# Kernel tuning notes

Measured on AMD Instinct MI355X. Metric: run time of the kernel, lower is better.

The kernel has to match this reference:

```python
import jax, jax.numpy as jnp
import numpy as np

B, H, S, D = 4, 16, 2048, 128

def setup_inputs() -> dict:
    key = jax.random.key(0)
    kq, kk, kv = jax.random.split(key, 3)
    q = jax.random.normal(kq, (B, H, S, D), dtype=jnp.float32)
    k = jax.random.normal(kk, (B, H, S, D), dtype=jnp.float32)
    v = jax.random.normal(kv, (B, H, S, D), dtype=jnp.float32)
    # causal mask: True = masked (upper triangle above the diagonal)
    mask = jnp.triu(jnp.ones((S, S), dtype=jnp.bool_), k=1)[None, None, :, :]
    return {"q": q, "k": k, "v": v, "mask": mask}

def reference(q, k, v, mask):
    head_dim = q.shape[-1]
    scale = 1.0 / jnp.sqrt(jnp.float32(head_dim))
    # scores: [B, H, Sq, Sk]
    scores = jnp.einsum('bhqd,bhkd->bhqk', q, k) * scale
    scores = jnp.where(mask, -jnp.inf, scores)
    attention_weights = jax.nn.softmax(scores, axis=-1)
    # dropout p=0.0 (eval): identity
    context_vectors = jnp.einsum('bhqk,bhkd->bhqd', attention_weights, v)
    return (context_vectors, attention_weights)
```

## Files before the change

kernel.cpp:

```cpp
#include <hip/hip_runtime.h>
#include <hip/hip_bf16.h>

#define S_LEN 2048
#define D_DIM 128
#define BH_N  64
#define BR    64
#define BC    64
#define NTILE (S_LEN / BC)
#define SCALE 0.08838834764831845f
#define SD    (S_LEN * D_DIM)
#define LSUM_BYTES (BH_N * S_LEN * 4)
#define WS_NEED (LSUM_BYTES + (size_t)BH_N * SD * 2)

typedef __attribute__((ext_vector_type(8)))  short short8;
typedef __attribute__((ext_vector_type(16))) float f32x16;
typedef __attribute__((ext_vector_type(4)))  float fv4;

__device__ __forceinline__ ushort f2bf(float f) {
  union { float f; unsigned u; } x; x.f = f;
  unsigned r = x.u + 0x7FFFu + ((x.u >> 16) & 1u);
  return (ushort)(r >> 16);
}

__device__ __forceinline__ short8 pack8(float4 a, float4 b) {
  short8 p;
  p[0] = (short)f2bf(a.x); p[1] = (short)f2bf(a.y);
  p[2] = (short)f2bf(a.z); p[3] = (short)f2bf(a.w);
  p[4] = (short)f2bf(b.x); p[5] = (short)f2bf(b.y);
  p[6] = (short)f2bf(b.z); p[7] = (short)f2bf(b.w);
  return p;
}

__global__ __launch_bounds__(256) void cvt_k_kernel(
    const float* __restrict__ k, ushort* __restrict__ kb) {
  size_t total = (size_t)BH_N * SD / 8;
  for (size_t i = (size_t)blockIdx.x * 256 + threadIdx.x; i < total;
       i += (size_t)gridDim.x * 256) {
    float4 a = *(const float4*)(k + i * 8);
    float4 b = *(const float4*)(k + i * 8 + 4);
    *(short8*)(kb + i * 8) = pack8(a, b);
  }
}

__device__ __forceinline__ void map_block_a(int bid, int& bh, int& qb) {
  int xcd  = bid & 7;
  int rest = bid >> 3;
  bh = (rest >> 5) * 8 + xcd;
  qb = (NTILE - 1) - (rest & 31);
}

template <bool KB16>
__global__ __launch_bounds__(256, 2) void attn_flash_kernel(
    const float* __restrict__ q, const float* __restrict__ k,
    const ushort* __restrict__ kb, const float* __restrict__ v,
    float* __restrict__ ctx, float* __restrict__ lsum_out) {
  __shared__ __align__(16) char klds[BC * 256];
  __shared__ __align__(16) char vtlds[D_DIM * 128];
  __shared__ __align__(16) char plds[BR * 128];
  __shared__ float lred[2][BR];

  const int tid  = threadIdx.x;
  const int lane = tid & 63;
  const int w    = tid >> 6;
  const int wq   = w >> 1, wk = w & 1;
  const int l31  = lane & 31, lhi = lane >> 5;

  int bh, qb;
  map_block_a(blockIdx.x, bh, qb);

  const float*  qbase  = q  + (size_t)bh * SD;
  const float*  kbase  = k  + (size_t)bh * SD;
  const ushort* kbbase = kb + (size_t)bh * SD;
  const float*  vbase  = v  + (size_t)bh * SD;

  short8 qf[8];
  {
    const float* qrow = qbase + (size_t)(qb * BR + wq * 32 + l31) * D_DIM;
    #pragma unroll
    for (int s = 0; s < 8; ++s) {
      int d0 = 16 * s + 8 * lhi;
      float4 a = *(const float4*)(qrow + d0);
      float4 b = *(const float4*)(qrow + d0 + 4);
      qf[s] = pack8(a, b);
    }
  }

  float4 kreg[8], vreg[8];
  short8 kreg16[4];

  auto load_k = [&](int kt) {
    int trow = tid >> 2, tc = tid & 3;
    if constexpr (KB16) {
      const ushort* src = kbbase + (size_t)(kt * BC + trow) * D_DIM;
      #pragma unroll
      for (int i = 0; i < 4; ++i)
        kreg16[i] = *(const short8*)(src + tc * 8 + i * 32);
    } else {
      const float* src = kbase + (size_t)(kt * BC + trow) * D_DIM;
      #pragma unroll
      for (int i = 0; i < 4; ++i) {
        int c0 = tc * 8 + i * 32;
        kreg[2 * i]     = *(const float4*)(src + c0);
        kreg[2 * i + 1] = *(const float4*)(src + c0 + 4);
      }
    }
  };
  auto write_k = [&]() {
    int trow = tid >> 2, tc = tid & 3;
    #pragma unroll
    for (int i = 0; i < 4; ++i) {
      int c0 = tc * 8 + i * 32;
      int off = (trow * 256 + c0 * 2) ^ ((trow & 7) << 4);
      if constexpr (KB16)
        *(short8*)(klds + off) = kreg16[i];
      else
        *(short8*)(klds + off) = pack8(kreg[2 * i], kreg[2 * i + 1]);
    }
  };
  auto load_v = [&](int kt) {
    int kp = tid & 31, dg = tid >> 5;
    const float* r0 = vbase + (size_t)(kt * BC + 2 * kp) * D_DIM + dg * 16;
    #pragma unroll
    for (int i = 0; i < 4; ++i) {
      vreg[i]     = *(const float4*)(r0 + 4 * i);
      vreg[4 + i] = *(const float4*)(r0 + D_DIM + 4 * i);
    }
  };
  auto write_v = [&]() {
    int kp = tid & 31, dg = tid >> 5;
    #pragma unroll
    for (int j = 0; j < 16; ++j) {
      int d = dg * 16 + j;
      float lo = vreg[j >> 2][j & 3];
      float hi = vreg[4 + (j >> 2)][j & 3];
      unsigned u = (unsigned)f2bf(lo) | ((unsigned)f2bf(hi) << 16);
      int off = (d * 128 + kp * 4) ^ ((d & 7) << 4);
      *(unsigned*)(vtlds + off) = u;
    }
  };

  auto compute_s = [&]() -> f32x16 {
    f32x16 acc;
    #pragma unroll
    for (int i = 0; i < 16; ++i) acc[i] = 0.f;
    int krow = wk * 32 + l31;
    int base = krow * 256;
    int swz  = (krow & 7) << 4;
    #pragma unroll
    for (int s = 0; s < 8; ++s) {
      int off = (base + 32 * s + 16 * lhi) ^ swz;
      short8 kf = *(const short8*)(klds + off);
      acc = __builtin_amdgcn_mfma_f32_32x32x16_bf16(qf[s], kf, acc, 0, 0, 0);
    }
    return acc;
  };

  float l_lane[16];
  f32x16 o0, o1;
  #pragma unroll
  for (int i = 0; i < 16; ++i) { l_lane[i] = 0.f; o0[i] = 0.f; o1[i] = 0.f; }

  load_k(0); load_v(0);

  for (int kt = 0; kt <= qb; ++kt) {
    write_k(); write_v();
    if (kt < qb) { load_k(kt + 1); load_v(kt + 1); }
    __syncthreads();

    f32x16 acc = compute_s();
    int kcol_l = wk * 32 + l31;
    int kcol = kt * BC + kcol_l;
    bool diag = (kt == qb);
    #pragma unroll
    for (int r = 0; r < 16; ++r) {
      int rl = wq * 32 + (r & 3) + 8 * (r >> 2) + 4 * lhi;
      int qrow = qb * BR + rl;
      float e = (diag && kcol > qrow) ? 0.f : __expf(acc[r] * SCALE);
      l_lane[r] += e;
      int poff = (rl * 128 + kcol_l * 2) ^ ((rl & 7) << 4);
      *(ushort*)(plds + poff) = f2bf(e);
    }
    __syncthreads();

    #pragma unroll
    for (int s = 0; s < 4; ++s) {
      int prow = wq * 32 + l31;
      int paoff = (prow * 128 + (16 * s + 8 * lhi) * 2) ^ ((prow & 7) << 4);
      short8 pa = *(const short8*)(plds + paoff);
      int kko = (16 * s + 8 * lhi) * 2;
      int d0 = wk * 64 + l31;
      int d1 = d0 + 32;
      int off0 = (d0 * 128 + kko) ^ ((d0 & 7) << 4);
      int off1 = (d1 * 128 + kko) ^ ((d1 & 7) << 4);
      short8 vb0 = *(const short8*)(vtlds + off0);
      short8 vb1 = *(const short8*)(vtlds + off1);
      o0 = __builtin_amdgcn_mfma_f32_32x32x16_bf16(pa, vb0, o0, 0, 0, 0);
      o1 = __builtin_amdgcn_mfma_f32_32x32x16_bf16(pa, vb1, o1, 0, 0, 0);
    }
    __syncthreads();
  }

  #pragma unroll
  for (int r = 0; r < 16; ++r) {
    float x = l_lane[r];
    x += __shfl_xor(x, 1);  x += __shfl_xor(x, 2);  x += __shfl_xor(x, 4);
    x += __shfl_xor(x, 8);  x += __shfl_xor(x, 16);
    l_lane[r] = x;
  }
  if (l31 == 0) {
    #pragma unroll
    for (int r = 0; r < 16; ++r) {
      int rl = wq * 32 + (r & 3) + 8 * (r >> 2) + 4 * lhi;
      lred[wk][rl] = l_lane[r];
    }
  }
  __syncthreads();

  if (tid < BR)
    lsum_out[(size_t)bh * S_LEN + qb * BR + tid] = lred[0][tid] + lred[1][tid];

  float inv_l[16];
  #pragma unroll
  for (int r = 0; r < 16; ++r) {
    int rl = wq * 32 + (r & 3) + 8 * (r >> 2) + 4 * lhi;
    inv_l[r] = 1.0f / (lred[0][rl] + lred[1][rl]);
  }
  #pragma unroll
  for (int r = 0; r < 16; ++r) {
    int rl = wq * 32 + (r & 3) + 8 * (r >> 2) + 4 * lhi;
    size_t obase = (size_t)(bh * S_LEN + qb * BR + rl) * D_DIM;
    ctx[obase + wk * 64 + l31]      = o0[r] * inv_l[r];
    ctx[obase + wk * 64 + 32 + l31] = o1[r] * inv_l[r];
  }
}

template <bool KB16>
__global__ __launch_bounds__(256) void attn_wts_stream_kernel(
    const float* __restrict__ q, const float* __restrict__ k,
    const ushort* __restrict__ kb, const float* __restrict__ lsum,
    float* __restrict__ wts) {
  const int tid  = threadIdx.x;
  const int lane = tid & 63;
  const int w    = tid >> 6;
  const int l31  = lane & 31, lhi = lane >> 5;

  int bh, panel;
  {
    int bid = blockIdx.x;
    int xcd = bid & 7, rest = bid >> 3;
    bh    = (rest >> 4) * 8 + xcd;
    panel = 15 - (rest & 15);
  }

  const int qrow0 = panel * 128 + w * 32;
  float* wbase = wts + ((size_t)bh * S_LEN + qrow0) * S_LEN;

  short8 qf[8];
  {
    const float* qrow = q + ((size_t)bh * S_LEN + qrow0 + l31) * D_DIM;
    #pragma unroll
    for (int s = 0; s < 8; ++s) {
      int d0 = 16 * s + 8 * lhi;
      float4 a = *(const float4*)(qrow + d0);
      float4 b = *(const float4*)(qrow + d0 + 4);
      qf[s] = pack8(a, b);
    }
  }

  float invl[16];
  #pragma unroll
  for (int r = 0; r < 16; ++r) {
    int rl = (r & 3) + 8 * (r >> 2) + 4 * lhi;
    invl[r] = 1.0f / lsum[(size_t)bh * S_LEN + qrow0 + rl];
  }

  const int qmax = qrow0 + 31;
  const int nkt  = qmax / 64 + 1;

  const ushort* kbb = kb + (size_t)bh * SD;
  const float*  kfb = k  + (size_t)bh * SD;

  for (int kt = 0; kt < nkt; ++kt) {
    f32x16 a0, a1;
    #pragma unroll
    for (int i = 0; i < 16; ++i) { a0[i] = 0.f; a1[i] = 0.f; }

    if constexpr (KB16) {
      const ushort* k0 = kbb + (size_t)(kt * 64 + l31) * D_DIM;
      const ushort* k1 = k0 + 32 * D_DIM;
      #pragma unroll
      for (int s8 = 0; s8 < 8; ++s8) {
        int d0 = 16 * s8 + 8 * lhi;
        short8 kf0 = *(const short8*)(k0 + d0);
        short8 kf1 = *(const short8*)(k1 + d0);
        a0 = __builtin_amdgcn_mfma_f32_32x32x16_bf16(qf[s8], kf0, a0, 0, 0, 0);
        a1 = __builtin_amdgcn_mfma_f32_32x32x16_bf16(qf[s8], kf1, a1, 0, 0, 0);
      }
    } else {
      const float* k0 = kfb + (size_t)(kt * 64 + l31) * D_DIM;
      const float* k1 = k0 + 32 * D_DIM;
      #pragma unroll
      for (int s8 = 0; s8 < 8; ++s8) {
        int d0 = 16 * s8 + 8 * lhi;
        short8 kf0 = pack8(*(const float4*)(k0 + d0), *(const float4*)(k0 + d0 + 4));
        short8 kf1 = pack8(*(const float4*)(k1 + d0), *(const float4*)(k1 + d0 + 4));
        a0 = __builtin_amdgcn_mfma_f32_32x32x16_bf16(qf[s8], kf0, a0, 0, 0, 0);
        a1 = __builtin_amdgcn_mfma_f32_32x32x16_bf16(qf[s8], kf1, a1, 0, 0, 0);
      }
    }

    const int kc0 = kt * 64 + l31;
    const int kc1 = kc0 + 32;
    #pragma unroll
    for (int r = 0; r < 16; ++r) {
      int qr = qrow0 + (r & 3) + 8 * (r >> 2) + 4 * lhi;
      a0[r] = (kc0 > qr) ? 0.f : __expf(a0[r] * SCALE) * invl[r];
      a1[r] = (kc1 > qr) ? 0.f : __expf(a1[r] * SCALE) * invl[r];
    }

    float* cbase = wbase + kt * 64 + lane;
    #pragma unroll
    for (int r = 0; r < 16; ++r) {
      float sA = __shfl(a1[r], lane ^ 32);
      float sB = __shfl(a0[r], lane ^ 32);
      float vA = lhi ? sA : a0[r];
      float vB = lhi ? a1[r] : sB;
      int rA = (r & 3) + 8 * (r >> 2);
      __builtin_nontemporal_store(vA, cbase + (size_t)rA * S_LEN);
      __builtin_nontemporal_store(vB, cbase + (size_t)(rA + 4) * S_LEN);
    }
  }

  fv4 z = (fv4)0.f;
  const int c0 = nkt * 64;
  for (int rr = 0; rr < 32; ++rr) {
    float* rowp = wbase + (size_t)rr * S_LEN;
    for (int c = c0 + lane * 4; c < S_LEN; c += 256)
      __builtin_nontemporal_store(z, (fv4*)(rowp + c));
  }
}

extern "C" void kernel_launch(void* const* d_in, const int* in_sizes, int n_in,
                              void* d_out, int out_size, void* d_ws, size_t ws_size,
                              hipStream_t stream) {
  const float* q = (const float*)d_in[0];
  const float* k = (const float*)d_in[1];
  const float* v = (const float*)d_in[2];
  float* ctx = (float*)d_out;
  float* wts = ctx + (size_t)BH_N * SD;
  float*  lsum = (float*)d_ws;
  ushort* kb16 = (ushort*)((char*)d_ws + LSUM_BYTES);

  const bool fast = ws_size >= WS_NEED;

  if (fast) {
    cvt_k_kernel<<<dim3(2048), dim3(256), 0, stream>>>(k, kb16);
    attn_flash_kernel<true><<<dim3(BH_N * NTILE), dim3(256), 0, stream>>>(
        q, k, kb16, v, ctx, lsum);
    attn_wts_stream_kernel<true><<<dim3(BH_N * 16), dim3(256), 0, stream>>>(
        q, k, kb16, lsum, wts);
  } else {
    attn_flash_kernel<false><<<dim3(BH_N * NTILE), dim3(256), 0, stream>>>(
        q, k, kb16, v, ctx, lsum);
    attn_wts_stream_kernel<false><<<dim3(BH_N * 16), dim3(256), 0, stream>>>(
        q, k, kb16, lsum, wts);
  }
}
```

Measured before the change: 560.8 us.

## Fuse flash context pass and weights streaming pass into one kernel per panel

Merges the flash-attention context kernel and the attention-weights streaming kernel into a single kernel. Each block handles a 128-row query panel with one warp per 32 rows, computes row sums and context first, then reuses the in-register Q fragments and row sums to write normalized weights. This removes the lsum workspace round-trip, one launch, and the second Q load. In exchange, each warp now computes all 64 key columns per tile, and the grid shrinks from 2048 to 1024 blocks, which lowers parallelism and can load-imbalance the causal panels.

```diff
diff --git a/kernel.cpp b/kernel.cpp
--- a/kernel.cpp
+++ b/kernel.cpp
@@ -4,13 +4,10 @@
 #define S_LEN 2048
 #define D_DIM 128
 #define BH_N  64
-#define BR    64
-#define BC    64
-#define NTILE (S_LEN / BC)
+#define NTILE 32
 #define SCALE 0.08838834764831845f
 #define SD    (S_LEN * D_DIM)
-#define LSUM_BYTES (BH_N * S_LEN * 4)
-#define WS_NEED (LSUM_BYTES + (size_t)BH_N * SD * 2)
+#define WS_NEED ((size_t)BH_N * SD * 2)
 
 typedef __attribute__((ext_vector_type(8)))  short short8;
 typedef __attribute__((ext_vector_type(16))) float f32x16;
@@ -42,40 +39,37 @@
   }
 }
 
-__device__ __forceinline__ void map_block_a(int bid, int& bh, int& qb) {
-  int xcd  = bid & 7;
-  int rest = bid >> 3;
-  bh = (rest >> 5) * 8 + xcd;
-  qb = (NTILE - 1) - (rest & 31);
-}
-
 template <bool KB16>
-__global__ __launch_bounds__(256, 2) void attn_flash_kernel(
+__global__ __launch_bounds__(256, 2) void attn_fused2_kernel(
     const float* __restrict__ q, const float* __restrict__ k,
     const ushort* __restrict__ kb, const float* __restrict__ v,
-    float* __restrict__ ctx, float* __restrict__ lsum_out) {
-  __shared__ __align__(16) char klds[BC * 256];
-  __shared__ __align__(16) char vtlds[D_DIM * 128];
-  __shared__ __align__(16) char plds[BR * 128];
-  __shared__ float lred[2][BR];
+    float* __restrict__ ctx, float* __restrict__ wts) {
+  __shared__ __align__(16) char klds[64 * 256];
+  __shared__ __align__(16) char vtlds[128 * 128];
+  __shared__ __align__(16) char plds[4 * 4096];
 
   const int tid  = threadIdx.x;
   const int lane = tid & 63;
   const int w    = tid >> 6;
-  const int wq   = w >> 1, wk = w & 1;
   const int l31  = lane & 31, lhi = lane >> 5;
 
-  int bh, qb;
-  map_block_a(blockIdx.x, bh, qb);
-
-  const float*  qbase  = q  + (size_t)bh * SD;
+  int bh, panel;
+  {
+    int bid = blockIdx.x;
+    int xcd = bid & 7, rest = bid >> 3;
+    bh    = (rest >> 4) * 8 + xcd;
+    panel = 15 - (rest & 15);
+  }
+  const int qrow0 = panel * 128 + w * 32;
+  char* pw = plds + w * 4096;
+
   const float*  kbase  = k  + (size_t)bh * SD;
   const ushort* kbbase = kb + (size_t)bh * SD;
   const float*  vbase  = v  + (size_t)bh * SD;
 
   short8 qf[8];
   {
-    const float* qrow = qbase + (size_t)(qb * BR + wq * 32 + l31) * D_DIM;
+    const float* qrow = q + ((size_t)bh * S_LEN + qrow0 + l31) * D_DIM;
     #pragma unroll
     for (int s = 0; s < 8; ++s) {
       int d0 = 16 * s + 8 * lhi;
@@ -91,12 +85,12 @@
   auto load_k = [&](int kt) {
     int trow = tid >> 2, tc = tid & 3;
     if constexpr (KB16) {
-      const ushort* src = kbbase + (size_t)(kt * BC + trow) * D_DIM;
+      const ushort* src = kbbase + (size_t)(kt * 64 + trow) * D_DIM;
       #pragma unroll
       for (int i = 0; i < 4; ++i)
         kreg16[i] = *(const short8*)(src + tc * 8 + i * 32);
     } else {
-      const float* src = kbase + (size_t)(kt * BC + trow) * D_DIM;
+      const float* src = kbase + (size_t)(kt * 64 + trow) * D_DIM;
       #pragma unroll
       for (int i = 0; i < 4; ++i) {
         int c0 = tc * 8 + i * 32;
@@ -119,7 +113,7 @@
   };
   auto load_v = [&](int kt) {
     int kp = tid & 31, dg = tid >> 5;
-    const float* r0 = vbase + (size_t)(kt * BC + 2 * kp) * D_DIM + dg * 16;
+    const float* r0 = vbase + (size_t)(kt * 64 + 2 * kp) * D_DIM + dg * 16;
     #pragma unroll
     for (int i = 0; i < 4; ++i) {
       vreg[i]     = *(const float4*)(r0 + 4 * i);
@@ -139,146 +133,83 @@
     }
   };
 
-  auto compute_s = [&]() -> f32x16 {
-    f32x16 acc;
-    #pragma unroll
-    for (int i = 0; i < 16; ++i) acc[i] = 0.f;
-    int krow = wk * 32 + l31;
-    int base = krow * 256;
-    int swz  = (krow & 7) << 4;
-    #pragma unroll
-    for (int s = 0; s < 8; ++s) {
-      int off = (base + 32 * s + 16 * lhi) ^ swz;
-      short8 kf = *(const short8*)(klds + off);
-      acc = __builtin_amdgcn_mfma_f32_32x32x16_bf16(qf[s], kf, acc, 0, 0, 0);
-    }
-    return acc;
-  };
-
   float l_lane[16];
-  f32x16 o0, o1;
+  f32x16 o0, o1, o2, o3;
   #pragma unroll
-  for (int i = 0; i < 16; ++i) { l_lane[i] = 0.f; o0[i] = 0.f; o1[i] = 0.f; }
-
+  for (int i = 0; i < 16; ++i) {
+    l_lane[i] = 0.f; o0[i] = 0.f; o1[i] = 0.f; o2[i] = 0.f; o3[i] = 0.f;
+  }
+
+  const int nkt_blk = 2 * panel + 2;
   load_k(0); load_v(0);
 
-  for (int kt = 0; kt <= qb; ++kt) {
+  for (int kt = 0; kt < nkt_blk; ++kt) {
     write_k(); write_v();
-    if (kt < qb) { load_k(kt + 1); load_v(kt + 1); }
+    if (kt + 1 < nkt_blk) { load_k(kt + 1); load_v(kt + 1); }
     __syncthreads();
 
-    f32x16 acc = compute_s();
-    int kcol_l = wk * 32 + l31;
-    int kcol = kt * BC + kcol_l;
-    bool diag = (kt == qb);
-    #pragma unroll
-    for (int r = 0; r < 16; ++r) {
-      int rl = wq * 32 + (r & 3) + 8 * (r >> 2) + 4 * lhi;
-      int qrow = qb * BR + rl;
-      float e = (diag && kcol > qrow) ? 0.f : __expf(acc[r] * SCALE);
-      l_lane[r] += e;
-      int poff = (rl * 128 + kcol_l * 2) ^ ((rl & 7) << 4);
-      *(ushort*)(plds + poff) = f2bf(e);
+    if (kt * 64 <= qrow0 + 31) {
+      f32x16 a0, a1;
+      #pragma unroll
+      for (int i = 0; i < 16; ++i) { a0[i] = 0.f; a1[i] = 0.f; }
+      const int swz = (l31 & 7) << 4;
+      #pragma unroll
+      for (int s8 = 0; s8 < 8; ++s8) {
+        int c = 32 * s8 + 16 * lhi;
+        short8 kf0 = *(const short8*)(klds + ((l31 * 256 + c) ^ swz));
+        short8 kf1 = *(const short8*)(klds + (((l31 + 32) * 256 + c) ^ swz));
+        a0 = __builtin_amdgcn_mfma_f32_32x32x16_bf16(qf[s8], kf0, a0, 0, 0, 0);
+        a1 = __builtin_amdgcn_mfma_f32_32x32x16_bf16(qf[s8], kf1, a1, 0, 0, 0);
+      }
+      const int kc0 = kt * 64 + l31, kc1 = kc0 + 32;
+      #pragma unroll
+      for (int r = 0; r < 16; ++r) {
+        int rl = (r & 3) + 8 * (r >> 2) + 4 * lhi;
+        int qr = qrow0 + rl;
+        float e0 = (kc0 > qr) ? 0.f : __expf(a0[r] * SCALE);
+        float e1 = (kc1 > qr) ? 0.f : __expf(a1[r] * SCALE);
+        l_lane[r] += e0 + e1;
+        int swzr = (rl & 7) << 4;
+        *(ushort*)(pw + ((rl * 128 + l31 * 2) ^ swzr))      = f2bf(e0);
+        *(ushort*)(pw + ((rl * 128 + 64 + l31 * 2) ^ swzr)) = f2bf(e1);
+      }
+      #pragma unroll
+      for (int s = 0; s < 4; ++s) {
+        int kko = (16 * s + 8 * lhi) * 2;
+        short8 pa = *(const short8*)(pw + ((l31 * 128 + kko) ^ ((l31 & 7) << 4)));
+        short8 vb0 = *(const short8*)(vtlds + (((0 * 32 + l31) * 128 + kko) ^ ((l31 & 7) << 4)));
+        short8 vb1 = *(const short8*)(vtlds + (((1 * 32 + l31) * 128 + kko) ^ (((32 + l31) & 7) << 4)));
+        short8 vb2 = *(const short8*)(vtlds + (((2 * 32 + l31) * 128 + kko) ^ (((64 + l31) & 7) << 4)));
+        short8 vb3 = *(const short8*)(vtlds + (((3 * 32 + l31) * 128 + kko) ^ (((96 + l31) & 7) << 4)));
+        o0 = __builtin_amdgcn_mfma_f32_32x32x16_bf16(pa, vb0, o0, 0, 0, 0);
+        o1 = __builtin_amdgcn_mfma_f32_32x32x16_bf16(pa, vb1, o1, 0, 0, 0);
+        o2 = __builtin_amdgcn_mfma_f32_32x32x16_bf16(pa, vb2, o2, 0, 0, 0);
+        o3 = __builtin_amdgcn_mfma_f32_32x32x16_bf16(pa, vb3, o3, 0, 0, 0);
+      }
     }
     __syncthreads();
-
-    #pragma unroll
-    for (int s = 0; s < 4; ++s) {
-      int prow = wq * 32 + l31;
-      int paoff = (prow * 128 + (16 * s + 8 * lhi) * 2) ^ ((prow & 7) << 4);
-      short8 pa = *(const short8*)(plds + paoff);
-      int kko = (16 * s + 8 * lhi) * 2;
-      int d0 = wk * 64 + l31;
-      int d1 = d0 + 32;
-      int off0 = (d0 * 128 + kko) ^ ((d0 & 7) << 4);
-      int off1 = (d1 * 128 + kko) ^ ((d1 & 7) << 4);
-      short8 vb0 = *(const short8*)(vtlds + off0);
-      short8 vb1 = *(const short8*)(vtlds + off1);
-      o0 = __builtin_amdgcn_mfma_f32_32x32x16_bf16(pa, vb0, o0, 0, 0, 0);
-      o1 = __builtin_amdgcn_mfma_f32_32x32x16_bf16(pa, vb1, o1, 0, 0, 0);
-    }
-    __syncthreads();
-  }
-
+  }
+
+  float inv_l[16];
   #pragma unroll
   for (int r = 0; r < 16; ++r) {
     float x = l_lane[r];
     x += __shfl_xor(x, 1);  x += __shfl_xor(x, 2);  x += __shfl_xor(x, 4);
     x += __shfl_xor(x, 8);  x += __shfl_xor(x, 16);
-    l_lane[r] = x;
-  }
-  if (l31 == 0) {
-    #pragma unroll
-    for (int r = 0; r < 16; ++r) {
-      int rl = wq * 32 + (r & 3) + 8 * (r >> 2) + 4 * lhi;
-      lred[wk][rl] = l_lane[r];
-    }
-  }
-  __syncthreads();
-
-  if (tid < BR)
-    lsum_out[(size_t)bh * S_LEN + qb * BR + tid] = lred[0][tid] + lred[1][tid];
-
-  float inv_l[16];
-  #pragma unroll
-  for (int r = 0; r < 16; ++r) {
-    int rl = wq * 32 + (r & 3) + 8 * (r >> 2) + 4 * lhi;
-    inv_l[r] = 1.0f / (lred[0][rl] + lred[1][rl]);
-  }
-  #pragma unroll
-  for (int r = 0; r < 16; ++r) {
-    int rl = wq * 32 + (r & 3) + 8 * (r >> 2) + 4 * lhi;
-    size_t obase = (size_t)(bh * S_LEN + qb * BR + rl) * D_DIM;
-    ctx[obase + wk * 64 + l31]      = o0[r] * inv_l[r];
-    ctx[obase + wk * 64 + 32 + l31] = o1[r] * inv_l[r];
-  }
-}
-
-template <bool KB16>
-__global__ __launch_bounds__(256) void attn_wts_stream_kernel(
-    const float* __restrict__ q, const float* __restrict__ k,
-    const ushort* __restrict__ kb, const float* __restrict__ lsum,
-    float* __restrict__ wts) {
-  const int tid  = threadIdx.x;
-  const int lane = tid & 63;
-  const int w    = tid >> 6;
-  const int l31  = lane & 31, lhi = lane >> 5;
-
-  int bh, panel;
-  {
-    int bid = blockIdx.x;
-    int xcd = bid & 7, rest = bid >> 3;
-    bh    = (rest >> 4) * 8 + xcd;
-    panel = 15 - (rest & 15);
-  }
-
-  const int qrow0 = panel * 128 + w * 32;
-  float* wbase = wts + ((size_t)bh * S_LEN + qrow0) * S_LEN;
-
-  short8 qf[8];
-  {
-    const float* qrow = q + ((size_t)bh * S_LEN + qrow0 + l31) * D_DIM;
-    #pragma unroll
-    for (int s = 0; s < 8; ++s) {
-      int d0 = 16 * s + 8 * lhi;
-      float4 a = *(const float4*)(qrow + d0);
-      float4 b = *(const float4*)(qrow + d0 + 4);
-      qf[s] = pack8(a, b);
-    }
-  }
-
-  float invl[16];
+    inv_l[r] = 1.0f / x;
+  }
   #pragma unroll
   for (int r = 0; r < 16; ++r) {
     int rl = (r & 3) + 8 * (r >> 2) + 4 * lhi;
-    invl[r] = 1.0f / lsum[(size_t)bh * S_LEN + qrow0 + rl];
-  }
-
-  const int qmax = qrow0 + 31;
-  const int nkt  = qmax / 64 + 1;
-
-  const ushort* kbb = kb + (size_t)bh * SD;
-  const float*  kfb = k  + (size_t)bh * SD;
+    float* cp = ctx + ((size_t)bh * S_LEN + qrow0 + rl) * D_DIM + l31;
+    cp[0]  = o0[r] * inv_l[r];
+    cp[32] = o1[r] * inv_l[r];
+    cp[64] = o2[r] * inv_l[r];
+    cp[96] = o3[r] * inv_l[r];
+  }
+
+  float* wbase = wts + ((size_t)bh * S_LEN + qrow0) * S_LEN;
+  const int nkt = (qrow0 + 31) / 64 + 1;
 
   for (int kt = 0; kt < nkt; ++kt) {
     f32x16 a0, a1;
@@ -286,7 +217,7 @@
     for (int i = 0; i < 16; ++i) { a0[i] = 0.f; a1[i] = 0.f; }
 
     if constexpr (KB16) {
-      const ushort* k0 = kbb + (size_t)(kt * 64 + l31) * D_DIM;
+      const ushort* k0 = kbbase + (size_t)(kt * 64 + l31) * D_DIM;
       const ushort* k1 = k0 + 32 * D_DIM;
       #pragma unroll
       for (int s8 = 0; s8 < 8; ++s8) {
@@ -297,7 +228,7 @@
         a1 = __builtin_amdgcn_mfma_f32_32x32x16_bf16(qf[s8], kf1, a1, 0, 0, 0);
       }
     } else {
-      const float* k0 = kfb + (size_t)(kt * 64 + l31) * D_DIM;
+      const float* k0 = kbase + (size_t)(kt * 64 + l31) * D_DIM;
       const float* k1 = k0 + 32 * D_DIM;
       #pragma unroll
       for (int s8 = 0; s8 < 8; ++s8) {
@@ -314,8 +245,8 @@
     #pragma unroll
     for (int r = 0; r < 16; ++r) {
       int qr = qrow0 + (r & 3) + 8 * (r >> 2) + 4 * lhi;
-      a0[r] = (kc0 > qr) ? 0.f : __expf(a0[r] * SCALE) * invl[r];
-      a1[r] = (kc1 > qr) ? 0.f : __expf(a1[r] * SCALE) * invl[r];
+      a0[r] = (kc0 > qr) ? 0.f : __expf(a0[r] * SCALE) * inv_l[r];
+      a1[r] = (kc1 > qr) ? 0.f : __expf(a1[r] * SCALE) * inv_l[r];
     }
 
     float* cbase = wbase + kt * 64 + lane;
@@ -348,21 +279,15 @@
   const float* v = (const float*)d_in[2];
   float* ctx = (float*)d_out;
   float* wts = ctx + (size_t)BH_N * SD;
-  float*  lsum = (float*)d_ws;
-  ushort* kb16 = (ushort*)((char*)d_ws + LSUM_BYTES);
+  ushort* kb16 = (ushort*)d_ws;
 
   const bool fast = ws_size >= WS_NEED;
-
   if (fast) {
     cvt_k_kernel<<<dim3(2048), dim3(256), 0, stream>>>(k, kb16);
-    attn_flash_kernel<true><<<dim3(BH_N * NTILE), dim3(256), 0, stream>>>(
-        q, k, kb16, v, ctx, lsum);
-    attn_wts_stream_kernel<true><<<dim3(BH_N * 16), dim3(256), 0, stream>>>(
-        q, k, kb16, lsum, wts);
+    attn_fused2_kernel<true><<<dim3(BH_N * 16), dim3(256), 0, stream>>>(
+        q, k, kb16, v, ctx, wts);
   } else {
-    attn_flash_kernel<false><<<dim3(BH_N * NTILE), dim3(256), 0, stream>>>(
-        q, k, kb16, v, ctx, lsum);
-    attn_wts_stream_kernel<false><<<dim3(BH_N * 16), dim3(256), 0, stream>>>(
-        q, k, kb16, lsum, wts);
-  }
-}
+    attn_fused2_kernel<false><<<dim3(BH_N * 16), dim3(256), 0, stream>>>(
+        q, k, kb16, v, ctx, wts);
+  }
+}
```

Measured after the change: 857.8 us. +53.0%, slower.

## Widen weights-stream kernel key tile to 256 columns per iteration

Applied to the files above, without the earlier changes.

The attention-weights streaming kernel now processes four 64-column key tiles (256 columns) per loop iteration, keeping eight MFMA accumulators live. All K loads and MFMAs for the group are issued before the exp/normalize and store phases, which exposes more memory-level parallelism and makes store bursts per row longer. The cost is much higher register pressure (128 accumulator floats), which can lower occupancy or cause spills. Masked-out tiles inside a group are still exp'd and stored as zeros, and the zero-fill tail now starts at a 256-aligned column. The BR macro was also replaced by the literal 64.

```diff
diff --git a/kernel.cpp b/kernel.cpp
--- a/kernel.cpp
+++ b/kernel.cpp
@@ -4,7 +4,6 @@
 #define S_LEN 2048
 #define D_DIM 128
 #define BH_N  64
-#define BR    64
 #define BC    64
 #define NTILE (S_LEN / BC)
 #define SCALE 0.08838834764831845f
@@ -56,8 +55,8 @@
     float* __restrict__ ctx, float* __restrict__ lsum_out) {
   __shared__ __align__(16) char klds[BC * 256];
   __shared__ __align__(16) char vtlds[D_DIM * 128];
-  __shared__ __align__(16) char plds[BR * 128];
-  __shared__ float lred[2][BR];
+  __shared__ __align__(16) char plds[64 * 128];
+  __shared__ float lred[2][64];
 
   const int tid  = threadIdx.x;
   const int lane = tid & 63;
@@ -75,7 +74,7 @@
 
   short8 qf[8];
   {
-    const float* qrow = qbase + (size_t)(qb * BR + wq * 32 + l31) * D_DIM;
+    const float* qrow = qbase + (size_t)(qb * 64 + wq * 32 + l31) * D_DIM;
     #pragma unroll
     for (int s = 0; s < 8; ++s) {
       int d0 = 16 * s + 8 * lhi;
@@ -174,7 +173,7 @@
     #pragma unroll
     for (int r = 0; r < 16; ++r) {
       int rl = wq * 32 + (r & 3) + 8 * (r >> 2) + 4 * lhi;
-      int qrow = qb * BR + rl;
+      int qrow = qb * 64 + rl;
       float e = (diag && kcol > qrow) ? 0.f : __expf(acc[r] * SCALE);
       l_lane[r] += e;
       int poff = (rl * 128 + kcol_l * 2) ^ ((rl & 7) << 4);
@@ -216,8 +215,8 @@
   }
   __syncthreads();
 
-  if (tid < BR)
-    lsum_out[(size_t)bh * S_LEN + qb * BR + tid] = lred[0][tid] + lred[1][tid];
+  if (tid < 64)
+    lsum_out[(size_t)bh * S_LEN + qb * 64 + tid] = lred[0][tid] + lred[1][tid];
 
   float inv_l[16];
   #pragma unroll
@@ -228,7 +227,7 @@
   #pragma unroll
   for (int r = 0; r < 16; ++r) {
     int rl = wq * 32 + (r & 3) + 8 * (r >> 2) + 4 * lhi;
-    size_t obase = (size_t)(bh * S_LEN + qb * BR + rl) * D_DIM;
+    size_t obase = (size_t)(bh * S_LEN + qb * 64 + rl) * D_DIM;
     ctx[obase + wk * 64 + l31]      = o0[r] * inv_l[r];
     ctx[obase + wk * 64 + 32 + l31] = o1[r] * inv_l[r];
   }
@@ -275,64 +274,83 @@
   }
 
   const int qmax = qrow0 + 31;
-  const int nkt  = qmax / 64 + 1;
+  const int nkg  = qmax / 256 + 1;
 
   const ushort* kbb = kb + (size_t)bh * SD;
   const float*  kfb = k  + (size_t)bh * SD;
 
-  for (int kt = 0; kt < nkt; ++kt) {
-    f32x16 a0, a1;
-    #pragma unroll
-    for (int i = 0; i < 16; ++i) { a0[i] = 0.f; a1[i] = 0.f; }
-
-    if constexpr (KB16) {
-      const ushort* k0 = kbb + (size_t)(kt * 64 + l31) * D_DIM;
-      const ushort* k1 = k0 + 32 * D_DIM;
-      #pragma unroll
-      for (int s8 = 0; s8 < 8; ++s8) {
-        int d0 = 16 * s8 + 8 * lhi;
-        short8 kf0 = *(const short8*)(k0 + d0);
-        short8 kf1 = *(const short8*)(k1 + d0);
-        a0 = __builtin_amdgcn_mfma_f32_32x32x16_bf16(qf[s8], kf0, a0, 0, 0, 0);
-        a1 = __builtin_amdgcn_mfma_f32_32x32x16_bf16(qf[s8], kf1, a1, 0, 0, 0);
-      }
-    } else {
-      const float* k0 = kfb + (size_t)(kt * 64 + l31) * D_DIM;
-      const float* k1 = k0 + 32 * D_DIM;
-      #pragma unroll
-      for (int s8 = 0; s8 < 8; ++s8) {
-        int d0 = 16 * s8 + 8 * lhi;
-        short8 kf0 = pack8(*(const float4*)(k0 + d0), *(const float4*)(k0 + d0 + 4));
-        short8 kf1 = pack8(*(const float4*)(k1 + d0), *(const float4*)(k1 + d0 + 4));
-        a0 = __builtin_amdgcn_mfma_f32_32x32x16_bf16(qf[s8], kf0, a0, 0, 0, 0);
-        a1 = __builtin_amdgcn_mfma_f32_32x32x16_bf16(qf[s8], kf1, a1, 0, 0, 0);
-      }
-    }
-
-    const int kc0 = kt * 64 + l31;
-    const int kc1 = kc0 + 32;
+  for (int kg = 0; kg < nkg; ++kg) {
+    f32x16 ac[8];
+    #pragma unroll
+    for (int t = 0; t < 8; ++t)
+      #pragma unroll
+      for (int i = 0; i < 16; ++i) ac[t][i] = 0.f;
+
+    #pragma unroll
+    for (int t = 0; t < 4; ++t) {
+      const int tc0 = kg * 256 + t * 64;
+      if (tc0 <= qmax) {
+        if constexpr (KB16) {
+          const ushort* k0 = kbb + (size_t)(tc0 + l31) * D_DIM;
+          const ushort* k1 = k0 + 32 * D_DIM;
+          #pragma unroll
+          for (int s8 = 0; s8 < 8; ++s8) {
+            int d0 = 16 * s8 + 8 * lhi;
+            short8 kf0 = *(const short8*)(k0 + d0);
+            short8 kf1 = *(const short8*)(k1 + d0);
+            ac[2 * t]     = __builtin_amdgcn_mfma_f32_32x32x16_bf16(qf[s8], kf0, ac[2 * t], 0, 0, 0);
+            ac[2 * t + 1] = __builtin_amdgcn_mfma_f32_32x32x16_bf16(qf[s8], kf1, ac[2 * t + 1], 0, 0, 0);
+          }
+        } else {
+          const float* k0 = kfb + (size_t)(tc0 + l31) * D_DIM;
+          const float* k1 = k0 + 32 * D_DIM;
+          #pragma unroll
+          for (int s8 = 0; s8 < 8; ++s8) {
+            int d0 = 16 * s8 + 8 * lhi;
+            short8 kf0 = pack8(*(const float4*)(k0 + d0), *(const float4*)(k0 + d0 + 4));
+            short8 kf1 = pack8(*(const float4*)(k1 + d0), *(const float4*)(k1 + d0 + 4));
+            ac[2 * t]     = __builtin_amdgcn_mfma_f32_32x32x16_bf16(qf[s8], kf0, ac[2 * t], 0, 0, 0);
+            ac[2 * t + 1] = __builtin_amdgcn_mfma_f32_32x32x16_bf16(qf[s8], kf1, ac[2 * t + 1], 0, 0, 0);
+          }
+        }
+      }
+    }
+
+    #pragma unroll
+    for (int t = 0; t < 4; ++t) {
+      const int kc0 = kg * 256 + t * 64 + l31;
+      const int kc1 = kc0 + 32;
+      #pragma unroll
+      for (int r = 0; r < 16; ++r) {
+        int qr = qrow0 + (r & 3) + 8 * (r >> 2) + 4 * lhi;
+        ac[2 * t][r]     = (kc0 > qr) ? 0.f : __expf(ac[2 * t][r] * SCALE) * invl[r];
+        ac[2 * t + 1][r] = (kc1 > qr) ? 0.f : __expf(ac[2 * t + 1][r] * SCALE) * invl[r];
+      }
+    }
+
+    float* gbase = wbase + kg * 256 + lane;
     #pragma unroll
     for (int r = 0; r < 16; ++r) {
-      int qr = qrow0 + (r & 3) + 8 * (r >> 2) + 4 * lhi;
-      a0[r] = (kc0 > qr) ? 0.f : __expf(a0[r] * SCALE) * invl[r];
-      a1[r] = (kc1 > qr) ? 0.f : __expf(a1[r] * SCALE) * invl[r];
-    }
-
-    float* cbase = wbase + kt * 64 + lane;
-    #pragma unroll
-    for (int r = 0; r < 16; ++r) {
-      float sA = __shfl(a1[r], lane ^ 32);
-      float sB = __shfl(a0[r], lane ^ 32);
-      float vA = lhi ? sA : a0[r];
-      float vB = lhi ? a1[r] : sB;
       int rA = (r & 3) + 8 * (r >> 2);
-      __builtin_nontemporal_store(vA, cbase + (size_t)rA * S_LEN);
-      __builtin_nontemporal_store(vB, cbase + (size_t)(rA + 4) * S_LEN);
+      float* rpA = gbase + (size_t)rA * S_LEN;
+      float* rpB = gbase + (size_t)(rA + 4) * S_LEN;
+      #pragma unroll
+      for (int t = 0; t < 4; ++t) {
+        float sA = __shfl(ac[2 * t + 1][r], lane ^ 32);
+        float vA = lhi ? sA : ac[2 * t][r];
+        __builtin_nontemporal_store(vA, rpA + t * 64);
+      }
+      #pragma unroll
+      for (int t = 0; t < 4; ++t) {
+        float sB = __shfl(ac[2 * t][r], lane ^ 32);
+        float vB = lhi ? ac[2 * t + 1][r] : sB;
+        __builtin_nontemporal_store(vB, rpB + t * 64);
+      }
     }
   }
 
   fv4 z = (fv4)0.f;
-  const int c0 = nkt * 64;
+  const int c0 = nkg * 256;
   for (int rr = 0; rr < 32; ++rr) {
     float* rowp = wbase + (size_t)rr * S_LEN;
     for (int c = c0 + lane * 4; c < S_LEN; c += 256)
```

Result: faster. 540.1 us (median of 2 runs) (-3.7%).
